# Kernel optimization log

Hardware: AMD Instinct MI355X
Metric: run time of the kernel (lower is better)

## Reference

```python
import jax, jax.numpy as jnp
import numpy as np

N_NODES = 50000
N_EDGES = 800000
IN_FEATS = 128
OUT_FEATS = 128
HEADS = 2
EW_DIMS = 2
NEG_SLOPE = 0.2


def setup_inputs() -> dict:
    key = jax.random.key(0)
    ks = jax.random.split(key, 8)
    feat = jax.random.normal(ks[0], (N_NODES, IN_FEATS), dtype=jnp.float32)
    e_w = jax.random.uniform(ks[1], (N_EDGES, EW_DIMS), dtype=jnp.float32)
    src = jax.random.randint(ks[2], (N_EDGES,), 0, N_NODES)
    dst = jax.random.randint(ks[3], (N_EDGES,), 0, N_NODES)
    # Learned params: per-head fc weight, attn vectors (xavier-ish scale)
    s = 1.0 / np.sqrt(IN_FEATS)
    W = jax.random.normal(ks[4], (HEADS, OUT_FEATS, IN_FEATS), dtype=jnp.float32) * s
    attn_l = jax.random.normal(ks[5], (HEADS, OUT_FEATS), dtype=jnp.float32) * s
    attn_r = jax.random.normal(ks[6], (HEADS, OUT_FEATS), dtype=jnp.float32) * s
    attn_ew = jax.random.normal(ks[7], (HEADS, EW_DIMS), dtype=jnp.float32)
    return {"feat": feat, "e_w": e_w, "src": src, "dst": dst,
            "W": W, "attn_l": attn_l, "attn_r": attn_r, "attn_ew": attn_ew}


def reference(feat, e_w, src, dst, W, attn_l, attn_r, attn_ew):
    N = feat.shape[0]
    # per-head projection: [N, H, O]
    ft = jnp.einsum('nf,hof->nho', feat, W)
    el = jnp.einsum('nho,ho->nh', ft, attn_l)           # [N, H]
    er = jnp.einsum('nho,ho->nh', ft, attn_r)           # [N, H]
    ew = jnp.einsum('ed,hd->eh', e_w, attn_ew)          # [E, H]
    # u_add_v + edge-weight attention + leaky_relu
    e = jax.nn.leaky_relu(el[src] + er[dst] + ew, NEG_SLOPE)  # [E, H]
    # edge_softmax grouped by destination node (numerically stable)
    emax = jax.ops.segment_max(e, dst, num_segments=N)
    emax = jnp.where(jnp.isfinite(emax), emax, 0.0)
    ee = jnp.exp(e - emax[dst])
    denom = jax.ops.segment_sum(ee, dst, num_segments=N)
    a = ee / jnp.where(denom[dst] > 0, denom[dst], 1.0)       # [E, H]
    # u_mul_e / sum aggregation: [N, H, O]
    m = ft[src] * a[:, :, None]
    rst = jax.ops.segment_sum(m, dst, num_segments=N)
    # residual (Identity since in_feats == out_feats) + elu, then cat heads
    rst = jax.nn.elu(rst + feat[:, None, :])
    return rst.reshape(N, -1)
```

## Files before the change

### kernel.cpp

```cpp
#include <hip/hip_runtime.h>
#include <math.h>

#define NNODES 50000
#define NEDGES 800000
#define INF 128
#define OUTF 128
#define HEADS 2
#define NEG_SLOPE 0.2f

#define CAP 32
#define OVFCAP 32768

__device__ __forceinline__ unsigned short f2bf(float f) {
    unsigned u = __float_as_uint(f);
    unsigned r = (u + 0x7FFFu + ((u >> 16) & 1u)) >> 16;
    return (unsigned short)r;
}
__device__ __forceinline__ float bf2f(unsigned short b) {
    return __uint_as_float((unsigned)b << 16);
}

typedef __attribute__((ext_vector_type(8))) short frag_ab;
typedef __attribute__((ext_vector_type(4))) float frag_cd;
typedef __attribute__((ext_vector_type(8))) unsigned short ushort8v;

__global__ void init_kernel(int* cursor, int* ovfcnt,
                            const float* __restrict__ W,
                            const float* __restrict__ attn_l,
                            const float* __restrict__ attn_r,
                            unsigned short* __restrict__ Wb,
                            float* __restrict__ wfold, int N) {
    const int b = blockIdx.x, t = threadIdx.x;
    const int cblk = (N + 255) >> 8;
    if (b < cblk) {
        int i = b * 256 + t;
        if (i < N) cursor[i] = 0;
        if (i == 0) *ovfcnt = 0;
        return;
    }
    if (b == cblk) {
        int h = t >> 7, f = t & 127;
        float sl = 0.f, sr = 0.f;
#pragma unroll 16
        for (int o = 0; o < 128; ++o) {
            float wv = W[(size_t)(h * 128 + o) * 128 + f];
            sl = fmaf(attn_l[h * 128 + o], wv, sl);
            sr = fmaf(attn_r[h * 128 + o], wv, sr);
        }
        wfold[h * 128 + f] = sl;
        wfold[(2 + h) * 128 + f] = sr;
        return;
    }
    int base = (b - cblk - 1) * 4096 + t * 16;
#pragma unroll
    for (int q = 0; q < 4; ++q) {
        float4 g = *(const float4*)(W + base + q * 4);
        ushort4 v; v.x = f2bf(g.x); v.y = f2bf(g.y); v.z = f2bf(g.z); v.w = f2bf(g.w);
        *(ushort4*)(Wb + base + q * 4) = v;
    }
}

__global__ __launch_bounds__(256) void gemm_mfma(const float* __restrict__ feat,
                                                 const unsigned short* __restrict__ Wb,
                                                 const float* __restrict__ wfold,
                                                 unsigned short* __restrict__ ftb,
                                                 float* __restrict__ el,
                                                 float* __restrict__ er,
                                                 int N) {
    const int t = threadIdx.x;
    const int w = t >> 6, lane = t & 63;
    const int m16 = lane & 15, quad = lane >> 4;
    const int n0 = blockIdx.x * 64;
    const int r = n0 + w * 16 + m16;
    const bool valid = r < N;

    frag_ab af[4];
    float pd[4] = {0.f, 0.f, 0.f, 0.f};
#pragma unroll
    for (int kc = 0; kc < 4; ++kc) {
        const int cc = kc * 32 + quad * 8;
        float4 g0 = make_float4(0.f, 0.f, 0.f, 0.f), g1 = g0;
        if (valid) {
            g0 = *(const float4*)(feat + (size_t)r * INF + cc);
            g1 = *(const float4*)(feat + (size_t)r * INF + cc + 4);
        }
        frag_ab a;
        a[0] = (short)f2bf(g0.x); a[1] = (short)f2bf(g0.y);
        a[2] = (short)f2bf(g0.z); a[3] = (short)f2bf(g0.w);
        a[4] = (short)f2bf(g1.x); a[5] = (short)f2bf(g1.y);
        a[6] = (short)f2bf(g1.z); a[7] = (short)f2bf(g1.w);
        af[kc] = a;
#pragma unroll
        for (int vq = 0; vq < 4; ++vq) {
            float4 w0 = *(const float4*)(wfold + vq * 128 + cc);
            float4 w1 = *(const float4*)(wfold + vq * 128 + cc + 4);
            pd[vq] += g0.x * w0.x + g0.y * w0.y + g0.z * w0.z + g0.w * w0.w
                    + g1.x * w1.x + g1.y * w1.y + g1.z * w1.z + g1.w * w1.w;
        }
    }
#pragma unroll
    for (int m = 16; m < 64; m <<= 1)
#pragma unroll
        for (int vq = 0; vq < 4; ++vq) pd[vq] += __shfl_xor(pd[vq], m, 64);
    if (valid && quad == 0) {
        *(float2*)(el + (size_t)r * 2) = make_float2(pd[0], pd[1]);
        *(float2*)(er + (size_t)r * 2) = make_float2(pd[2], pd[3]);
    }

#pragma unroll 1
    for (int jt = 0; jt < 4; ++jt) {
        frag_ab bfr[16];
#pragma unroll
        for (int kc = 0; kc < 4; ++kc)
#pragma unroll
            for (int nt = 0; nt < 4; ++nt)
                bfr[kc * 4 + nt] = *(const frag_ab*)(Wb
                        + (size_t)(jt * 64 + nt * 16 + m16) * INF + kc * 32 + quad * 8);

        frag_cd acc[4];
#pragma unroll
        for (int nt = 0; nt < 4; ++nt) acc[nt] = frag_cd{0.f, 0.f, 0.f, 0.f};
#pragma unroll
        for (int kc = 0; kc < 4; ++kc)
#pragma unroll
            for (int nt = 0; nt < 4; ++nt)
                acc[nt] = __builtin_amdgcn_mfma_f32_16x16x32_bf16(af[kc], bfr[kc * 4 + nt],
                                                                  acc[nt], 0, 0, 0);
#pragma unroll
        for (int nt = 0; nt < 4; ++nt) {
            const int gj = jt * 64 + nt * 16 + m16;
#pragma unroll
            for (int reg = 0; reg < 4; ++reg) {
                int gm = n0 + w * 16 + quad * 4 + reg;
                if (gm < N) ftb[(size_t)gm * 256 + gj] = f2bf(acc[nt][reg]);
            }
        }
    }
}

__global__ void edge_fused(const float* __restrict__ el, const float* __restrict__ er,
                           const float* __restrict__ e_w, const int* __restrict__ src,
                           const int* __restrict__ dst, const float* __restrict__ attn_ew,
                           int* __restrict__ cursor, int* __restrict__ ovfcnt,
                           uint2* __restrict__ edata, float4* __restrict__ ovf,
                           int E) {
    int e = blockIdx.x * 256 + threadIdx.x;
    if (e >= E) return;
    int s = src[e], d = dst[e];
    float2 ew2 = *(const float2*)(e_w + (size_t)e * 2);
    float2 elv = *(const float2*)(el + (size_t)s * 2);
    float2 erv = *(const float2*)(er + (size_t)d * 2);
    float v0 = elv.x + erv.x + ew2.x * attn_ew[0] + ew2.y * attn_ew[1];
    float v1 = elv.y + erv.y + ew2.x * attn_ew[2] + ew2.y * attn_ew[3];
    v0 = v0 >= 0.f ? v0 : NEG_SLOPE * v0;
    v1 = v1 >= 0.f ? v1 : NEG_SLOPE * v1;
    float ee0 = __expf(v0);
    float ee1 = __expf(v1);
    int pos = atomicAdd(cursor + d, 1);
    if (pos < CAP) {
        unsigned pk = ((unsigned)f2bf(ee1) << 16) | (unsigned)f2bf(ee0);
        edata[(size_t)d * CAP + pos] = make_uint2((unsigned)s, pk);
    } else {
        int o = atomicAdd(ovfcnt, 1);
        if (o < OVFCAP)
            ovf[o] = make_float4(__int_as_float(d), __int_as_float(s), ee0, ee1);
    }
}

__global__ __launch_bounds__(256) void aggregate(const unsigned short* __restrict__ ftb,
                                                 const float* __restrict__ feat,
                                                 const uint2* __restrict__ edata,
                                                 const int* __restrict__ cursor,
                                                 const int* __restrict__ ovfcnt,
                                                 const float4* __restrict__ ovf,
                                                 float* __restrict__ out, int N) {
    const int t = threadIdx.x;
    const int w = t >> 6, l = t & 63;
    const int n = blockIdx.x * 4 + w;
    if (n >= N) return;
    const int hl = l & 31;
    const int half = l >> 5;
    const int c8 = 8 * hl;
    const int h = hl >> 4;
    const int cnt = cursor[n];
    const int cmain = cnt < CAP ? cnt : CAP;
    const uint2* eb = edata + (size_t)n * CAP;

    float4 a0 = make_float4(0.f, 0.f, 0.f, 0.f);
    float4 a1 = make_float4(0.f, 0.f, 0.f, 0.f);
    float dn = 0.f;
    const int hm = (cmain + 1) >> 1;
#pragma unroll 4
    for (int i = 0; i < hm; ++i) {
        const int j = 2 * i + half;
        const bool vld = j < cmain;
        uint2 rec = eb[vld ? j : 0];
        float aw = bf2f((unsigned short)(h ? (rec.y >> 16) : (rec.y & 0xFFFFu)));
        float a = vld ? aw : 0.f;
        unsigned su = vld ? rec.x : 0u;
        ushort8v v = *(const ushort8v*)(ftb + (size_t)su * 256 + c8);
        dn += a;
        a0.x = fmaf(a, bf2f(v[0]), a0.x);
        a0.y = fmaf(a, bf2f(v[1]), a0.y);
        a0.z = fmaf(a, bf2f(v[2]), a0.z);
        a0.w = fmaf(a, bf2f(v[3]), a0.w);
        a1.x = fmaf(a, bf2f(v[4]), a1.x);
        a1.y = fmaf(a, bf2f(v[5]), a1.y);
        a1.z = fmaf(a, bf2f(v[6]), a1.z);
        a1.w = fmaf(a, bf2f(v[7]), a1.w);
    }
    a0.x += __shfl_xor(a0.x, 32, 64);
    a0.y += __shfl_xor(a0.y, 32, 64);
    a0.z += __shfl_xor(a0.z, 32, 64);
    a0.w += __shfl_xor(a0.w, 32, 64);
    a1.x += __shfl_xor(a1.x, 32, 64);
    a1.y += __shfl_xor(a1.y, 32, 64);
    a1.z += __shfl_xor(a1.z, 32, 64);
    a1.w += __shfl_xor(a1.w, 32, 64);
    dn += __shfl_xor(dn, 32, 64);

    if (cnt > CAP) {
        int no = *ovfcnt; if (no > OVFCAP) no = OVFCAP;
        for (int i = 0; i < no; ++i) {
            float4 ov = ovf[i];
            if (__float_as_int(ov.x) == n) {
                int s = __float_as_int(ov.y);
                float a = h ? ov.w : ov.z;
                dn += a;
                ushort8v v = *(const ushort8v*)(ftb + (size_t)s * 256 + c8);
                a0.x = fmaf(a, bf2f(v[0]), a0.x);
                a0.y = fmaf(a, bf2f(v[1]), a0.y);
                a0.z = fmaf(a, bf2f(v[2]), a0.z);
                a0.w = fmaf(a, bf2f(v[3]), a0.w);
                a1.x = fmaf(a, bf2f(v[4]), a1.x);
                a1.y = fmaf(a, bf2f(v[5]), a1.y);
                a1.z = fmaf(a, bf2f(v[6]), a1.z);
                a1.w = fmaf(a, bf2f(v[7]), a1.w);
            }
        }
    }
    float inv = dn > 0.f ? 1.0f / dn : 0.f;
    const int cb = c8 + 4 * half;
    float4 av = half ? a1 : a0;
    float4 f4 = *(const float4*)(feat + (size_t)n * INF + (cb & 127));
    float4 r;
    r.x = fmaf(av.x, inv, f4.x);
    r.y = fmaf(av.y, inv, f4.y);
    r.z = fmaf(av.z, inv, f4.z);
    r.w = fmaf(av.w, inv, f4.w);
    r.x = r.x > 0.f ? r.x : expm1f(r.x);
    r.y = r.y > 0.f ? r.y : expm1f(r.y);
    r.z = r.z > 0.f ? r.z : expm1f(r.z);
    r.w = r.w > 0.f ? r.w : expm1f(r.w);
    *(float4*)(out + (size_t)n * 256 + cb) = r;
}

extern "C" void kernel_launch(void* const* d_in, const int* in_sizes, int n_in,
                              void* d_out, int out_size, void* d_ws, size_t ws_size,
                              hipStream_t stream) {
    const float* feat    = (const float*)d_in[0];
    const float* e_w     = (const float*)d_in[1];
    const int*   src     = (const int*)d_in[2];
    const int*   dst     = (const int*)d_in[3];
    const float* W       = (const float*)d_in[4];
    const float* attn_l  = (const float*)d_in[5];
    const float* attn_r  = (const float*)d_in[6];
    const float* attn_ew = (const float*)d_in[7];
    float* out = (float*)d_out;

    const int N = in_sizes[0] / INF;
    const int E = in_sizes[2];

    unsigned short* ftb = (unsigned short*)d_ws;
    uint2*  edata  = (uint2*)(ftb + (size_t)N * 256);
    float*  el     = (float*)(edata + (size_t)N * CAP);
    float*  er     = el + (size_t)N * 2;
    float*  wfold  = er + (size_t)N * 2;
    unsigned short* Wb = (unsigned short*)(wfold + 512);
    float4* ovf    = (float4*)(Wb + 32768);
    int*    cursor = (int*)(ovf + OVFCAP);
    int*    ovfcnt = cursor + N;

    const int cblk = (N + 255) / 256;
    init_kernel<<<cblk + 9, 256, 0, stream>>>(cursor, ovfcnt, W, attn_l, attn_r, Wb, wfold, N);

    gemm_mfma<<<(N + 63) / 64, 256, 0, stream>>>(feat, Wb, wfold, ftb, el, er, N);

    edge_fused<<<(E + 255) / 256, 256, 0, stream>>>(el, er, e_w, src, dst, attn_ew,
                                                    cursor, ovfcnt, edata, ovf, E);

    aggregate<<<(N + 3) / 4, 256, 0, stream>>>(ftb, feat, edata, cursor, ovfcnt, ovf, out, N);
}
```

Before: 241.4 us.

## Stage W in LDS for GEMM and split per-node edge cursors into two sub-bins

The GEMM kernel now copies the whole bf16 weight matrix into padded shared memory once per block and reads B fragments from LDS, where before each wave reloaded them from global memory, and the jt loop is fully unrolled. The edge kernel splits each node's 32-slot bin into two 16-slot halves, each with its own atomic cursor selected by edge parity, and falls back to the other half and then to the overflow list. This is meant to halve contention on each destination's atomic counter. The cost is about 68KB of LDS per GEMM block, which lowers occupancy, plus extra index arithmetic in aggregate.

```diff
diff --git a/kernel.cpp b/kernel.cpp
--- a/kernel.cpp
+++ b/kernel.cpp
@@ -9,6 +9,7 @@
 #define NEG_SLOPE 0.2f
 
 #define CAP 32
+#define SCAP 16
 #define OVFCAP 32768
 
 __device__ __forceinline__ unsigned short f2bf(float f) {
@@ -23,6 +24,8 @@
 typedef __attribute__((ext_vector_type(8))) short frag_ab;
 typedef __attribute__((ext_vector_type(4))) float frag_cd;
 typedef __attribute__((ext_vector_type(8))) unsigned short ushort8v;
+
+#define APITCH 136
 
 __global__ void init_kernel(int* cursor, int* ovfcnt,
                             const float* __restrict__ W,
@@ -31,14 +34,14 @@
                             unsigned short* __restrict__ Wb,
                             float* __restrict__ wfold, int N) {
     const int b = blockIdx.x, t = threadIdx.x;
-    const int cblk = (N + 255) >> 8;
-    if (b < cblk) {
+    const int czblk = (2 * N + 255) >> 8;
+    if (b < czblk) {
         int i = b * 256 + t;
-        if (i < N) cursor[i] = 0;
+        if (i < 2 * N) cursor[i] = 0;
         if (i == 0) *ovfcnt = 0;
         return;
     }
-    if (b == cblk) {
+    if (b == czblk) {
         int h = t >> 7, f = t & 127;
         float sl = 0.f, sr = 0.f;
 #pragma unroll 16
@@ -51,7 +54,7 @@
         wfold[(2 + h) * 128 + f] = sr;
         return;
     }
-    int base = (b - cblk - 1) * 4096 + t * 16;
+    int base = (b - czblk - 1) * 4096 + t * 16;
 #pragma unroll
     for (int q = 0; q < 4; ++q) {
         float4 g = *(const float4*)(W + base + q * 4);
@@ -67,6 +70,7 @@
                                                  float* __restrict__ el,
                                                  float* __restrict__ er,
                                                  int N) {
+    __shared__ unsigned short Bs[256 * APITCH];
     const int t = threadIdx.x;
     const int w = t >> 6, lane = t & 63;
     const int m16 = lane & 15, quad = lane >> 4;
@@ -74,6 +78,14 @@
     const int r = n0 + w * 16 + m16;
     const bool valid = r < N;
 
+#pragma unroll
+    for (int i = 0; i < 16; ++i) {
+        int q = t + i * 256;
+        int row = q >> 4, c = q & 15;
+        ushort8v v = *(const ushort8v*)(Wb + row * 128 + c * 8);
+        *(ushort8v*)(&Bs[row * APITCH + c * 8]) = v;
+    }
+
     frag_ab af[4];
     float pd[4] = {0.f, 0.f, 0.f, 0.f};
 #pragma unroll
@@ -107,25 +119,21 @@
         *(float2*)(er + (size_t)r * 2) = make_float2(pd[2], pd[3]);
     }
 
-#pragma unroll 1
+    __syncthreads();
+
+#pragma unroll
     for (int jt = 0; jt < 4; ++jt) {
-        frag_ab bfr[16];
+        frag_cd acc[4];
+#pragma unroll
+        for (int nt = 0; nt < 4; ++nt) acc[nt] = frag_cd{0.f, 0.f, 0.f, 0.f};
 #pragma unroll
         for (int kc = 0; kc < 4; ++kc)
 #pragma unroll
-            for (int nt = 0; nt < 4; ++nt)
-                bfr[kc * 4 + nt] = *(const frag_ab*)(Wb
-                        + (size_t)(jt * 64 + nt * 16 + m16) * INF + kc * 32 + quad * 8);
-
-        frag_cd acc[4];
-#pragma unroll
-        for (int nt = 0; nt < 4; ++nt) acc[nt] = frag_cd{0.f, 0.f, 0.f, 0.f};
-#pragma unroll
-        for (int kc = 0; kc < 4; ++kc)
-#pragma unroll
-            for (int nt = 0; nt < 4; ++nt)
-                acc[nt] = __builtin_amdgcn_mfma_f32_16x16x32_bf16(af[kc], bfr[kc * 4 + nt],
-                                                                  acc[nt], 0, 0, 0);
+            for (int nt = 0; nt < 4; ++nt) {
+                frag_ab bf = *(const frag_ab*)(&Bs[(jt * 64 + nt * 16 + m16) * APITCH
+                                                   + kc * 32 + quad * 8]);
+                acc[nt] = __builtin_amdgcn_mfma_f32_16x16x32_bf16(af[kc], bf, acc[nt], 0, 0, 0);
+            }
 #pragma unroll
         for (int nt = 0; nt < 4; ++nt) {
             const int gj = jt * 64 + nt * 16 + m16;
@@ -143,7 +151,7 @@
                            const int* __restrict__ dst, const float* __restrict__ attn_ew,
                            int* __restrict__ cursor, int* __restrict__ ovfcnt,
                            uint2* __restrict__ edata, float4* __restrict__ ovf,
-                           int E) {
+                           int N, int E) {
     int e = blockIdx.x * 256 + threadIdx.x;
     if (e >= E) return;
     int s = src[e], d = dst[e];
@@ -156,14 +164,23 @@
     v1 = v1 >= 0.f ? v1 : NEG_SLOPE * v1;
     float ee0 = __expf(v0);
     float ee1 = __expf(v1);
-    int pos = atomicAdd(cursor + d, 1);
-    if (pos < CAP) {
-        unsigned pk = ((unsigned)f2bf(ee1) << 16) | (unsigned)f2bf(ee0);
-        edata[(size_t)d * CAP + pos] = make_uint2((unsigned)s, pk);
+    unsigned pk = ((unsigned)f2bf(ee1) << 16) | (unsigned)f2bf(ee0);
+    uint2 rec = make_uint2((unsigned)s, pk);
+    uint2* bin = edata + (size_t)d * CAP;
+    int sh = e & 1;
+    int pos = atomicAdd(cursor + (size_t)sh * N + d, 1);
+    if (pos < SCAP) {
+        bin[sh * SCAP + pos] = rec;
     } else {
-        int o = atomicAdd(ovfcnt, 1);
-        if (o < OVFCAP)
-            ovf[o] = make_float4(__int_as_float(d), __int_as_float(s), ee0, ee1);
+        sh ^= 1;
+        int pos2 = atomicAdd(cursor + (size_t)sh * N + d, 1);
+        if (pos2 < SCAP) {
+            bin[sh * SCAP + pos2] = rec;
+        } else {
+            int o = atomicAdd(ovfcnt, 1);
+            if (o < OVFCAP)
+                ovf[o] = make_float4(__int_as_float(d), __int_as_float(s), ee0, ee1);
+        }
     }
 }
 
@@ -182,19 +199,22 @@
     const int half = l >> 5;
     const int c8 = 8 * hl;
     const int h = hl >> 4;
-    const int cnt = cursor[n];
-    const int cmain = cnt < CAP ? cnt : CAP;
+    const int c0c = cursor[n], c1c = cursor[N + n];
+    const int cnt0 = c0c < SCAP ? c0c : SCAP;
+    const int cnt1 = c1c < SCAP ? c1c : SCAP;
+    const int cnt = cnt0 + cnt1;
     const uint2* eb = edata + (size_t)n * CAP;
 
     float4 a0 = make_float4(0.f, 0.f, 0.f, 0.f);
     float4 a1 = make_float4(0.f, 0.f, 0.f, 0.f);
     float dn = 0.f;
-    const int hm = (cmain + 1) >> 1;
-#pragma unroll 4
+    const int hm = (cnt + 1) >> 1;
+#pragma unroll 8
     for (int i = 0; i < hm; ++i) {
         const int j = 2 * i + half;
-        const bool vld = j < cmain;
-        uint2 rec = eb[vld ? j : 0];
+        const bool vld = j < cnt;
+        const int jj = j < cnt0 ? j : j - cnt0 + SCAP;
+        uint2 rec = eb[vld ? jj : 0];
         float aw = bf2f((unsigned short)(h ? (rec.y >> 16) : (rec.y & 0xFFFFu)));
         float a = vld ? aw : 0.f;
         unsigned su = vld ? rec.x : 0u;
@@ -219,7 +239,7 @@
     a1.w += __shfl_xor(a1.w, 32, 64);
     dn += __shfl_xor(dn, 32, 64);
 
-    if (cnt > CAP) {
+    if (c0c > SCAP && c1c > SCAP) {
         int no = *ovfcnt; if (no > OVFCAP) no = OVFCAP;
         for (int i = 0; i < no; ++i) {
             float4 ov = ovf[i];
@@ -279,15 +299,15 @@
     unsigned short* Wb = (unsigned short*)(wfold + 512);
     float4* ovf    = (float4*)(Wb + 32768);
     int*    cursor = (int*)(ovf + OVFCAP);
-    int*    ovfcnt = cursor + N;
-
-    const int cblk = (N + 255) / 256;
-    init_kernel<<<cblk + 9, 256, 0, stream>>>(cursor, ovfcnt, W, attn_l, attn_r, Wb, wfold, N);
+    int*    ovfcnt = cursor + 2 * (size_t)N;
+
+    const int czblk = (2 * N + 255) / 256;
+    init_kernel<<<czblk + 9, 256, 0, stream>>>(cursor, ovfcnt, W, attn_l, attn_r, Wb, wfold, N);
 
     gemm_mfma<<<(N + 63) / 64, 256, 0, stream>>>(feat, Wb, wfold, ftb, el, er, N);
 
     edge_fused<<<(E + 255) / 256, 256, 0, stream>>>(el, er, e_w, src, dst, attn_ew,
-                                                    cursor, ovfcnt, edata, ovf, E);
+                                                    cursor, ovfcnt, edata, ovf, N, E);
 
     aggregate<<<(N + 3) / 4, 256, 0, stream>>>(ftb, feat, edata, cursor, ovfcnt, ovf, out, N);
 }
```

New measurement: 224.6 us. -7.0%, faster.
